# Optimization experiments

Hardware: AMD Instinct MI355X
Metric: run time of the kernel (lower is better)

The kernel has to match this reference:

```python
import jax, jax.numpy as jnp
import numpy as np

D_MODEL = 768
CTX_DIM = 1024
N_HEAD = 12
N_QUERIES = 256
DIM_HEAD = D_MODEL // N_HEAD  # 64
INNER = DIM_HEAD * N_HEAD     # 768
EPS = 1e-5


def layernorm(x, w, b):
    mu = jnp.mean(x, axis=-1, keepdims=True)
    var = jnp.mean((x - mu) ** 2, axis=-1, keepdims=True)
    return (x - mu) * jax.lax.rsqrt(var + EPS) * w + b


def setup_inputs() -> dict:
    key = jax.random.key(0)
    ks = jax.random.split(key, 9)
    x = jax.random.normal(ks[0], (8, 4096, CTX_DIM), dtype=jnp.float32)
    query = jax.random.normal(ks[1], (N_QUERIES, D_MODEL), dtype=jnp.float32)
    # Linear weights stored [in, out] (y = x @ W)
    Wq = jax.random.normal(ks[2], (D_MODEL, INNER), dtype=jnp.float32) * 0.02
    Wkv = jax.random.normal(ks[3], (CTX_DIM, 2 * INNER), dtype=jnp.float32) * 0.02
    Wout = jax.random.normal(ks[4], (INNER, D_MODEL), dtype=jnp.float32) * 0.02
    ln_q_w = jnp.ones((D_MODEL,), jnp.float32)
    ln_q_b = jnp.zeros((D_MODEL,), jnp.float32)
    ln_k_w = jnp.ones((CTX_DIM,), jnp.float32)
    ln_k_b = jnp.zeros((CTX_DIM,), jnp.float32)
    return {"x": x, "query": query, "ln_q_w": ln_q_w, "ln_q_b": ln_q_b,
            "ln_k_w": ln_k_w, "ln_k_b": ln_k_b, "Wq": Wq, "Wkv": Wkv, "Wout": Wout}


def reference(x, query, ln_q_w, ln_q_b, ln_k_w, ln_k_b, Wq, Wkv, Wout):
    b = x.shape[0]
    h, dh = N_HEAD, DIM_HEAD
    scale = dh ** -0.5
    xk = x[:, None]  # b 1 n d  (m = 1)
    m, n = xk.shape[1], xk.shape[2]
    q = jnp.broadcast_to(query, (b, m) + query.shape)  # b m nq d
    xk = layernorm(xk, ln_k_w, ln_k_b)
    q = layernorm(q, ln_q_w, ln_q_b)
    q = q @ Wq                          # b m nq inner
    kv = xk @ Wkv                       # b m n 2*inner
    k, v = jnp.split(kv, 2, axis=-1)
    def split_heads(t):
        bb, tt, nn, _ = t.shape
        return t.reshape(bb, tt, nn, h, dh).transpose(0, 3, 1, 2, 4)  # b h t n dh
    q, k, v = split_heads(q), split_heads(k), split_heads(v)
    sim = jnp.einsum('bhtid,bhtjd->bhtij', q * scale, k)
    attn = jax.nn.softmax(sim, axis=-1)
    out = jnp.einsum('bhtij,bhtjd->bhtid', attn, v)  # b h t nq dh
    out = out.transpose(0, 2, 3, 1, 4).reshape(b, m, N_QUERIES, INNER)
    return (out @ Wout).squeeze(axis=1)  # b nq d_model
```

## Files before the change

### kernel.cpp

```cpp
#include <hip/hip_runtime.h>
#include <hip/hip_bf16.h>
#include <math.h>

#define B_    8
#define T_    4096
#define CD    1024
#define DM    768
#define NH    12
#define DH    64
#define NQ    256
#define INNER 768
#define NKV   1536
#define MKV   (B_*T_)
#define EPS   1e-5f
#define SCALE 0.125f

typedef __attribute__((ext_vector_type(8))) short short8;
typedef __attribute__((ext_vector_type(4))) float f32x4;

__device__ __forceinline__ unsigned short f2bf(float f) {
  union { __hip_bfloat16 h; unsigned short u; } cv;
  cv.h = __float2bfloat16(f);
  return cv.u;
}
__device__ __forceinline__ float bf2f(unsigned short u) {
  return __uint_as_float(((unsigned int)u) << 16);
}

__global__ __launch_bounds__(256) void tbw_kernel(
    const float* __restrict__ s0, unsigned short* __restrict__ d0,
    const float* __restrict__ s1, unsigned short* __restrict__ d1,
    const float* __restrict__ s2, unsigned short* __restrict__ d2) {
  int z = blockIdx.z;
  const float* src; unsigned short* dst; int SR, SC;
  if (z == 0)      { src = s0; dst = d0; SR = CD;    SC = NKV; }
  else if (z == 1) { src = s1; dst = d1; SR = DM;    SC = INNER; }
  else             { src = s2; dst = d2; SR = INNER; SC = DM; }
  int k0 = blockIdx.x * 32, n0 = blockIdx.y * 32;
  if (k0 >= SR || n0 >= SC) return;
  __shared__ float tile[32][33];
  int tid = threadIdx.x;
  int r = tid >> 3, c4 = (tid & 7) * 4;
  float4 v = *reinterpret_cast<const float4*>(&src[(size_t)(k0 + r) * SC + n0 + c4]);
  tile[r][c4 + 0] = v.x; tile[r][c4 + 1] = v.y; tile[r][c4 + 2] = v.z; tile[r][c4 + 3] = v.w;
  __syncthreads();
  ushort4 o4;
  o4.x = f2bf(tile[c4 + 0][r]);
  o4.y = f2bf(tile[c4 + 1][r]);
  o4.z = f2bf(tile[c4 + 2][r]);
  o4.w = f2bf(tile[c4 + 3][r]);
  *reinterpret_cast<ushort4*>(&dst[(size_t)(n0 + r) * SR + k0 + c4]) = o4;
}

__global__ __launch_bounds__(256) void qln_kernel(
    const float* __restrict__ query, const float* __restrict__ lnw,
    const float* __restrict__ lnb, unsigned short* __restrict__ qn) {
  int row = blockIdx.x, tid = threadIdx.x;
  __shared__ float rbuf[256];
  const float* qr = query + (size_t)row * DM;
  float v0 = qr[tid], v1 = qr[tid + 256], v2 = qr[tid + 512];
  rbuf[tid] = v0 + v1 + v2;
  __syncthreads();
  for (int o = 128; o > 0; o >>= 1) { if (tid < o) rbuf[tid] += rbuf[tid + o]; __syncthreads(); }
  float mean = rbuf[0] * (1.f / 768.f);
  __syncthreads();
  float d0 = v0 - mean, d1 = v1 - mean, d2 = v2 - mean;
  rbuf[tid] = d0 * d0 + d1 * d1 + d2 * d2;
  __syncthreads();
  for (int o = 128; o > 0; o >>= 1) { if (tid < o) rbuf[tid] += rbuf[tid + o]; __syncthreads(); }
  float var = rbuf[0] * (1.f / 768.f);
  float rs = rsqrtf(var + EPS);
  unsigned short* dst = qn + (size_t)row * DM;
  dst[tid]       = f2bf(d0 * rs * lnw[tid]       + lnb[tid]);
  dst[tid + 256] = f2bf(d1 * rs * lnw[tid + 256] + lnb[tid + 256]);
  dst[tid + 512] = f2bf(d2 * rs * lnw[tid + 512] + lnb[tid + 512]);
}

__global__ __launch_bounds__(256) void xnorm_kernel(
    const float* __restrict__ x, const float* __restrict__ lnw,
    const float* __restrict__ lnb, unsigned short* __restrict__ xn) {
  int row = blockIdx.x, tid = threadIdx.x;
  float4 v = reinterpret_cast<const float4*>(x + (size_t)row * CD)[tid];
  float s  = v.x + v.y + v.z + v.w;
  float ss = v.x * v.x + v.y * v.y + v.z * v.z + v.w * v.w;
  #pragma unroll
  for (int o = 32; o > 0; o >>= 1) { s += __shfl_down(s, o); ss += __shfl_down(ss, o); }
  __shared__ float sm[8];
  int wid = tid >> 6, lane = tid & 63;
  if (lane == 0) { sm[wid] = s; sm[4 + wid] = ss; }
  __syncthreads();
  float S  = sm[0] + sm[1] + sm[2] + sm[3];
  float SS = sm[4] + sm[5] + sm[6] + sm[7];
  float m  = S * (1.f / 1024.f);
  float var = SS * (1.f / 1024.f) - m * m;
  float rs = rsqrtf(fmaxf(var, 0.f) + EPS);
  float4 wv = reinterpret_cast<const float4*>(lnw)[tid];
  float4 bv = reinterpret_cast<const float4*>(lnb)[tid];
  ushort4 o4;
  o4.x = f2bf((v.x - m) * rs * wv.x + bv.x);
  o4.y = f2bf((v.y - m) * rs * wv.y + bv.y);
  o4.z = f2bf((v.z - m) * rs * wv.z + bv.z);
  o4.w = f2bf((v.w - m) * rs * wv.w + bv.w);
  reinterpret_cast<ushort4*>(xn + (size_t)row * CD)[tid] = o4;
}

template <int MODE>
__global__ __launch_bounds__(256) void gemm128_kernel(
    const unsigned short* __restrict__ A, const unsigned short* __restrict__ Bt,
    void* __restrict__ Cout, int N, int K, int nN, float scale, int swz) {
  __shared__ __attribute__((aligned(16))) unsigned short As[128 * 64];
  __shared__ __attribute__((aligned(16))) unsigned short Bs[128 * 64];
  int tid = threadIdx.x;
  int w = tid >> 6, lane = tid & 63;
  int bid = blockIdx.x;
  int sw = swz ? ((bid & 7) * ((int)gridDim.x >> 3) + (bid >> 3)) : bid;
  int mt = sw / nN, nt = sw % nN;
  int m0 = mt * 128, n0 = nt * 128;

  int srow[4], skoff[4];
  #pragma unroll
  for (int i = 0; i < 4; ++i) {
    int L = w * 4096 + i * 1024 + lane * 16;
    int row = L >> 7;
    int slot = (L >> 4) & 7;
    srow[i] = row;
    skoff[i] = ((slot ^ (row & 7)) << 3);
  }

  f32x4 acc[4][4];
  #pragma unroll
  for (int m = 0; m < 4; ++m)
    #pragma unroll
    for (int n = 0; n < 4; ++n) acc[m][n] = (f32x4){0.f, 0.f, 0.f, 0.f};

  int wr = w >> 1, wc = w & 1;
  int l15 = lane & 15, l4 = lane >> 4;

  for (int t = 0; t < K / 64; ++t) {
    int k0 = t * 64;
    #pragma unroll
    for (int i = 0; i < 4; ++i) {
      __builtin_amdgcn_global_load_lds(
          (const __attribute__((address_space(1))) void*)(A + (size_t)(m0 + srow[i]) * K + k0 + skoff[i]),
          (__attribute__((address_space(3))) void*)(As + w * 2048 + i * 512 + lane * 8),
          16, 0, 0);
    }
    #pragma unroll
    for (int i = 0; i < 4; ++i) {
      __builtin_amdgcn_global_load_lds(
          (const __attribute__((address_space(1))) void*)(Bt + (size_t)(n0 + srow[i]) * K + k0 + skoff[i]),
          (__attribute__((address_space(3))) void*)(Bs + w * 2048 + i * 512 + lane * 8),
          16, 0, 0);
    }
    __syncthreads();
    #pragma unroll
    for (int kh = 0; kh < 2; ++kh) {
      short8 af[4], bf[4];
      #pragma unroll
      for (int m = 0; m < 4; ++m) {
        int row = wr * 64 + m * 16 + l15;
        int byte = row * 128 + (((l4 + 4 * kh) ^ (row & 7)) << 4);
        af[m] = *reinterpret_cast<const short8*>(reinterpret_cast<const char*>(As) + byte);
      }
      #pragma unroll
      for (int n = 0; n < 4; ++n) {
        int row = wc * 64 + n * 16 + l15;
        int byte = row * 128 + (((l4 + 4 * kh) ^ (row & 7)) << 4);
        bf[n] = *reinterpret_cast<const short8*>(reinterpret_cast<const char*>(Bs) + byte);
      }
      #pragma unroll
      for (int m = 0; m < 4; ++m)
        #pragma unroll
        for (int n = 0; n < 4; ++n)
          acc[m][n] = __builtin_amdgcn_mfma_f32_16x16x32_bf16(af[m], bf[n], acc[m][n], 0, 0, 0);
    }
    __syncthreads();
  }

  #pragma unroll
  for (int m = 0; m < 4; ++m) {
    int grow = m0 + wr * 64 + m * 16 + l4 * 4;
    #pragma unroll
    for (int n = 0; n < 4; ++n) {
      int gcol = n0 + wc * 64 + n * 16 + l15;
      #pragma unroll
      for (int r = 0; r < 4; ++r) {
        if (MODE == 0)
          ((unsigned short*)Cout)[(size_t)(grow + r) * N + gcol] = f2bf(acc[m][n][r] * scale);
        else
          ((float*)Cout)[(size_t)(grow + r) * N + gcol] = acc[m][n][r];
      }
    }
  }
}

#define KBM 256
#define KBN 256
#define KBK 64
__global__ __launch_bounds__(512, 2) void kv_split_kernel(
    const unsigned short* __restrict__ xn, const unsigned short* __restrict__ wkvT,
    unsigned short* __restrict__ kvbK, unsigned short* __restrict__ vT) {
  __shared__ __attribute__((aligned(16))) unsigned short As[2][KBM * KBK];
  __shared__ __attribute__((aligned(16))) unsigned short Bs[2][KBN * KBK];
  int tid = threadIdx.x;
  int w = tid >> 6, lane = tid & 63;
  int wm = w >> 2, wn = w & 3;
  int l15 = lane & 15, l4 = lane >> 4;

  int bid = blockIdx.x;
  int sw = (bid & 7) * 96 + (bid >> 3);
  int mt = sw / (NKV / KBN), nt = sw % (NKV / KBN);
  int m0 = mt * KBM, n0 = nt * KBN;

  int srow[4], koff[4];
  #pragma unroll
  for (int i = 0; i < 4; ++i) {
    int r = i * 64 + (tid >> 3);
    srow[i] = r;
    koff[i] = (((tid & 7) ^ (r & 7)) << 3);
  }

  f32x4 acc[8][4];
  #pragma unroll
  for (int m = 0; m < 8; ++m)
    #pragma unroll
    for (int n = 0; n < 4; ++n) acc[m][n] = (f32x4){0.f, 0.f, 0.f, 0.f};

  #pragma unroll
  for (int i = 0; i < 4; ++i) {
    __builtin_amdgcn_global_load_lds(
        (const __attribute__((address_space(1))) void*)(xn + (size_t)(m0 + srow[i]) * CD + koff[i]),
        (__attribute__((address_space(3))) void*)(&As[0][0] + i * 4096 + tid * 8), 16, 0, 0);
    __builtin_amdgcn_global_load_lds(
        (const __attribute__((address_space(1))) void*)(wkvT + (size_t)(n0 + srow[i]) * CD + koff[i]),
        (__attribute__((address_space(3))) void*)(&Bs[0][0] + i * 4096 + tid * 8), 16, 0, 0);
  }
  __syncthreads();

  for (int t = 0; t < CD / KBK; ++t) {
    int cur = t & 1;
    if (t + 1 < CD / KBK) {
      int k0 = (t + 1) * KBK;
      #pragma unroll
      for (int i = 0; i < 4; ++i) {
        __builtin_amdgcn_global_load_lds(
            (const __attribute__((address_space(1))) void*)(xn + (size_t)(m0 + srow[i]) * CD + k0 + koff[i]),
            (__attribute__((address_space(3))) void*)(&As[cur ^ 1][0] + i * 4096 + tid * 8), 16, 0, 0);
        __builtin_amdgcn_global_load_lds(
            (const __attribute__((address_space(1))) void*)(wkvT + (size_t)(n0 + srow[i]) * CD + k0 + koff[i]),
            (__attribute__((address_space(3))) void*)(&Bs[cur ^ 1][0] + i * 4096 + tid * 8), 16, 0, 0);
      }
    }
    const char* Ab = reinterpret_cast<const char*>(&As[cur][0]);
    const char* Bb = reinterpret_cast<const char*>(&Bs[cur][0]);
    #pragma unroll
    for (int kh = 0; kh < 2; ++kh) {
      short8 bf[4];
      #pragma unroll
      for (int n = 0; n < 4; ++n) {
        int row = wn * 64 + n * 16 + l15;
        int byt = row * 128 + (((kh * 4 + l4) ^ (row & 7)) << 4);
        bf[n] = *reinterpret_cast<const short8*>(Bb + byt);
      }
      #pragma unroll
      for (int m = 0; m < 8; ++m) {
        int row = wm * 128 + m * 16 + l15;
        int byt = row * 128 + (((kh * 4 + l4) ^ (row & 7)) << 4);
        short8 af = *reinterpret_cast<const short8*>(Ab + byt);
        #pragma unroll
        for (int n = 0; n < 4; ++n)
          acc[m][n] = __builtin_amdgcn_mfma_f32_16x16x32_bf16(af, bf[n], acc[m][n], 0, 0, 0);
      }
    }
    __syncthreads();
  }

  if (nt < 3) {
    #pragma unroll
    for (int m = 0; m < 8; ++m) {
      int grow = m0 + wm * 128 + m * 16 + l4 * 4;
      #pragma unroll
      for (int n = 0; n < 4; ++n) {
        int gcol = nt * 256 + wn * 64 + n * 16 + l15;
        #pragma unroll
        for (int r = 0; r < 4; ++r)
          kvbK[(size_t)(grow + r) * INNER + gcol] = f2bf(acc[m][n][r]);
      }
    }
  } else {
    int b = m0 >> 12;
    int jblk = m0 & 4095;
    char* Asc = reinterpret_cast<char*>(&As[0][0]);
    char* Bsc = reinterpret_cast<char*>(&Bs[0][0]);
    char* tb = (wn < 2 ? Asc : Bsc) + (wn & 1) * 32768;
    #pragma unroll
    for (int m = 0; m < 8; ++m) {
      int off = (wm * 128 + m * 16 + l4 * 4) * 2;
      #pragma unroll
      for (int n = 0; n < 4; ++n) {
        int d = n * 16 + l15;
        ushort4 o4;
        o4.x = f2bf(acc[m][n][0]); o4.y = f2bf(acc[m][n][1]);
        o4.z = f2bf(acc[m][n][2]); o4.w = f2bf(acc[m][n][3]);
        *reinterpret_cast<ushort4*>(tb + d * 512 + (off ^ ((d & 7) << 4))) = o4;
      }
    }
    __syncthreads();
    #pragma unroll
    for (int e = 0; e < 16; ++e) {
      int lin = e * 8192 + tid * 16;
      int wnn = lin >> 15;
      int rem = lin & 32767;
      int d = rem >> 9;
      int inner = rem & 511;
      short8 v8 = *reinterpret_cast<const short8*>(
          (wnn < 2 ? Asc : Bsc) + (wnn & 1) * 32768 + d * 512 + (inner ^ ((d & 7) << 4)));
      int jl = inner >> 1;
      int hh = (nt - 3) * 4 + wnn;
      unsigned short* dst = vT + ((size_t)(b * NH + hh) * DH + d) * T_ + jblk + jl;
      *reinterpret_cast<short8*>(dst) = v8;
    }
  }
}

__global__ __launch_bounds__(256) void attn_mfma_kernel(
    const unsigned short* __restrict__ qpb, const unsigned short* __restrict__ kvbK,
    const unsigned short* __restrict__ vT,
    unsigned short* __restrict__ pOb, float* __restrict__ pM, float* __restrict__ pL) {
  int bh = blockIdx.x, kc = blockIdx.y, qt = blockIdx.z;
  int b = bh / NH, h = bh % NH;
  __shared__ __attribute__((aligned(16))) unsigned short Ks[2][4096];
  __shared__ __attribute__((aligned(16))) unsigned short Vs[2][4096];
  __shared__ __attribute__((aligned(16))) unsigned short Ps[4][1024];
  int tid = threadIdx.x;
  int w = tid >> 6, lane = tid & 63;
  int l15 = lane & 15, l4 = lane >> 4;

  short8 qf[2];
  {
    const unsigned short* qb = qpb + (size_t)(qt * 64 + w * 16 + l15) * INNER + h * DH;
    qf[0] = *reinterpret_cast<const short8*>(qb + l4 * 8);
    qf[1] = *reinterpret_cast<const short8*>(qb + 32 + l4 * 8);
  }

  int srow0 = w * 16 + (lane >> 3);
  int srow1 = srow0 + 8;
  int koff0 = (((lane & 7) ^ (srow0 & 7)) << 3);
  int koff1 = (((lane & 7) ^ (srow1 & 7)) << 3);

  const size_t kbase = ((size_t)b * T_) * INNER + h * DH;
  const size_t vbase = ((size_t)bh * DH) * T_;

  auto stageKV = [&](int kt, int d) {
    int j0 = kc * 2048 + kt * 64;
    __builtin_amdgcn_global_load_lds(
        (const __attribute__((address_space(1))) void*)(kvbK + kbase + (size_t)(j0 + srow0) * INNER + koff0),
        (__attribute__((address_space(3))) void*)(&Ks[d][0] + w * 1024 + lane * 8), 16, 0, 0);
    __builtin_amdgcn_global_load_lds(
        (const __attribute__((address_space(1))) void*)(kvbK + kbase + (size_t)(j0 + srow1) * INNER + koff1),
        (__attribute__((address_space(3))) void*)(&Ks[d][0] + w * 1024 + 512 + lane * 8), 16, 0, 0);
    __builtin_amdgcn_global_load_lds(
        (const __attribute__((address_space(1))) void*)(vT + vbase + (size_t)srow0 * T_ + j0 + koff0),
        (__attribute__((address_space(3))) void*)(&Vs[d][0] + w * 1024 + lane * 8), 16, 0, 0);
    __builtin_amdgcn_global_load_lds(
        (const __attribute__((address_space(1))) void*)(vT + vbase + (size_t)srow1 * T_ + j0 + koff1),
        (__attribute__((address_space(3))) void*)(&Vs[d][0] + w * 1024 + 512 + lane * 8), 16, 0, 0);
  };

  f32x4 o[4];
  #pragma unroll
  for (int i = 0; i < 4; ++i) o[i] = (f32x4){0.f, 0.f, 0.f, 0.f};
  float m_run = -1e30f, l_run = 0.f;

  stageKV(0, 0);

  for (int kt = 0; kt < 32; ++kt) {
    int cur = kt & 1;
    if (kt + 1 < 32) {
      stageKV(kt + 1, cur ^ 1);
      asm volatile("s_waitcnt vmcnt(4)" ::: "memory");
    } else {
      asm volatile("s_waitcnt vmcnt(0)" ::: "memory");
    }
    __builtin_amdgcn_s_barrier();
    __builtin_amdgcn_sched_barrier(0);

    const char* Kb = reinterpret_cast<const char*>(&Ks[cur][0]);
    const char* Vb = reinterpret_cast<const char*>(&Vs[cur][0]);

    f32x4 st[4];
    __builtin_amdgcn_s_setprio(1);
    #pragma unroll
    for (int sub = 0; sub < 4; ++sub) {
      st[sub] = (f32x4){0.f, 0.f, 0.f, 0.f};
      #pragma unroll
      for (int hf = 0; hf < 2; ++hf) {
        int row = sub * 16 + l15;
        int byt = row * 128 + (((l4 + 4 * hf) ^ (row & 7)) << 4);
        short8 kf = *reinterpret_cast<const short8*>(Kb + byt);
        st[sub] = __builtin_amdgcn_mfma_f32_16x16x32_bf16(kf, qf[hf], st[sub], 0, 0, 0);
      }
    }
    __builtin_amdgcn_s_setprio(0);

    float tmax = -1e30f;
    #pragma unroll
    for (int sub = 0; sub < 4; ++sub)
      #pragma unroll
      for (int r = 0; r < 4; ++r) tmax = fmaxf(tmax, st[sub][r]);
    tmax = fmaxf(tmax, __shfl_xor(tmax, 16));
    tmax = fmaxf(tmax, __shfl_xor(tmax, 32));

    if (__ballot(tmax > m_run + 8.f)) {
      float m_new = fmaxf(m_run, tmax);
      float alpha = __expf(m_run - m_new);
      float ao[4];
      #pragma unroll
      for (int r = 0; r < 4; ++r) ao[r] = __shfl(alpha, (l4 << 2) | r);
      #pragma unroll
      for (int ds = 0; ds < 4; ++ds)
        #pragma unroll
        for (int r = 0; r < 4; ++r) o[ds][r] *= ao[r];
      l_run *= alpha;
      m_run = m_new;
    }

    float psum = 0.f;
    #pragma unroll
    for (int sub = 0; sub < 4; ++sub) {
      float p0 = __expf(st[sub][0] - m_run);
      float p1 = __expf(st[sub][1] - m_run);
      float p2 = __expf(st[sub][2] - m_run);
      float p3 = __expf(st[sub][3] - m_run);
      psum += (p0 + p1) + (p2 + p3);
      unsigned int u0 = (unsigned int)f2bf(p0) | ((unsigned int)f2bf(p1) << 16);
      unsigned int u1 = (unsigned int)f2bf(p2) | ((unsigned int)f2bf(p3) << 16);
      int slot = (sub * 2 + (l4 >> 1)) ^ (l15 & 7);
      int byt = l15 * 128 + (slot << 4) + (l4 & 1) * 8;
      uint2 uv; uv.x = u0; uv.y = u1;
      *reinterpret_cast<uint2*>(reinterpret_cast<char*>(Ps[w]) + byt) = uv;
    }
    psum += __shfl_xor(psum, 16);
    psum += __shfl_xor(psum, 32);
    l_run += psum;

    short8 pa[2];
    #pragma unroll
    for (int hf = 0; hf < 2; ++hf) {
      int byt = l15 * 128 + ((((hf << 2) + l4) ^ (l15 & 7)) << 4);
      pa[hf] = *reinterpret_cast<const short8*>(reinterpret_cast<const char*>(Ps[w]) + byt);
    }
    __builtin_amdgcn_s_setprio(1);
    #pragma unroll
    for (int ds = 0; ds < 4; ++ds) {
      #pragma unroll
      for (int hf = 0; hf < 2; ++hf) {
        int row = ds * 16 + l15;
        int byt = row * 128 + (((l4 + 4 * hf) ^ (row & 7)) << 4);
        short8 vf = *reinterpret_cast<const short8*>(Vb + byt);
        o[ds] = __builtin_amdgcn_mfma_f32_16x16x32_bf16(pa[hf], vf, o[ds], 0, 0, 0);
      }
    }
    __builtin_amdgcn_s_setprio(0);
    __builtin_amdgcn_s_barrier();
    __builtin_amdgcn_sched_barrier(0);
  }

  int pidx = bh * 2 + kc;
  int qrow0 = qt * 64 + w * 16;
  if (l4 == 0) {
    pM[(size_t)pidx * NQ + qrow0 + l15] = m_run;
    pL[(size_t)pidx * NQ + qrow0 + l15] = l_run;
  }
  #pragma unroll
  for (int ds = 0; ds < 4; ++ds)
    #pragma unroll
    for (int r = 0; r < 4; ++r)
      pOb[((size_t)pidx * NQ + qrow0 + l4 * 4 + r) * DH + ds * 16 + l15] = f2bf(o[ds][r]);
}

__global__ __launch_bounds__(256) void outfuse_kernel(
    const unsigned short* __restrict__ pOb, const float* __restrict__ pM,
    const float* __restrict__ pL, const unsigned short* __restrict__ WoutT,
    float* __restrict__ out) {
  __shared__ __attribute__((aligned(16))) unsigned short As[128 * 64];
  __shared__ __attribute__((aligned(16))) unsigned short Bs[128 * 64];
  int tid = threadIdx.x;
  int w = tid >> 6, lane = tid & 63;
  int bid = blockIdx.x;
  int sw = (bid & 7) * 12 + (bid >> 3);
  int mt = sw / 6, nt = sw % 6;
  int m0 = mt * 128, n0 = nt * 128;

  int srow[4], skoff[4];
  #pragma unroll
  for (int i = 0; i < 4; ++i) {
    int L = w * 4096 + i * 1024 + lane * 16;
    int row = L >> 7;
    int slot = (L >> 4) & 7;
    srow[i] = row;
    skoff[i] = ((slot ^ (row & 7)) << 3);
  }

  f32x4 acc[4][4];
  #pragma unroll
  for (int m = 0; m < 4; ++m)
    #pragma unroll
    for (int n = 0; n < 4; ++n) acc[m][n] = (f32x4){0.f, 0.f, 0.f, 0.f};

  int wr = w >> 1, wc = w & 1;
  int l15 = lane & 15, l4 = lane >> 4;

  for (int t = 0; t < NH; ++t) {
    #pragma unroll
    for (int i = 0; i < 4; ++i) {
      int lin = i * 256 + tid;
      int r = lin >> 3, sl = lin & 7;
      int gr = m0 + r;
      int b = gr >> 8, q = gr & 255;
      size_t i0 = ((size_t)(b * NH + t) * 2) * NQ + q;
      size_t i1 = i0 + NQ;
      float m1 = pM[i0], m2 = pM[i1], l1 = pL[i0], l2 = pL[i1];
      float Mx = fmaxf(m1, m2);
      float w1 = __expf(m1 - Mx), w2 = __expf(m2 - Mx);
      float invL = 1.f / (l1 * w1 + l2 * w2);
      w1 *= invL; w2 *= invL;
      short8 s0 = *reinterpret_cast<const short8*>(pOb + i0 * DH + sl * 8);
      short8 s1 = *reinterpret_cast<const short8*>(pOb + i1 * DH + sl * 8);
      short8 v8;
      #pragma unroll
      for (int k = 0; k < 8; ++k)
        v8[k] = (short)f2bf(bf2f((unsigned short)s0[k]) * w1 +
                            bf2f((unsigned short)s1[k]) * w2);
      *reinterpret_cast<short8*>(reinterpret_cast<char*>(As) +
                                 r * 128 + ((sl ^ (r & 7)) << 4)) = v8;
    }
    int k0 = t * 64;
    #pragma unroll
    for (int i = 0; i < 4; ++i) {
      __builtin_amdgcn_global_load_lds(
          (const __attribute__((address_space(1))) void*)(WoutT + (size_t)(n0 + srow[i]) * INNER + k0 + skoff[i]),
          (__attribute__((address_space(3))) void*)(Bs + w * 2048 + i * 512 + lane * 8),
          16, 0, 0);
    }
    __syncthreads();
    #pragma unroll
    for (int kh = 0; kh < 2; ++kh) {
      short8 af[4], bf[4];
      #pragma unroll
      for (int m = 0; m < 4; ++m) {
        int row = wr * 64 + m * 16 + l15;
        int byte = row * 128 + (((l4 + 4 * kh) ^ (row & 7)) << 4);
        af[m] = *reinterpret_cast<const short8*>(reinterpret_cast<const char*>(As) + byte);
      }
      #pragma unroll
      for (int n = 0; n < 4; ++n) {
        int row = wc * 64 + n * 16 + l15;
        int byte = row * 128 + (((l4 + 4 * kh) ^ (row & 7)) << 4);
        bf[n] = *reinterpret_cast<const short8*>(reinterpret_cast<const char*>(Bs) + byte);
      }
      #pragma unroll
      for (int m = 0; m < 4; ++m)
        #pragma unroll
        for (int n = 0; n < 4; ++n)
          acc[m][n] = __builtin_amdgcn_mfma_f32_16x16x32_bf16(af[m], bf[n], acc[m][n], 0, 0, 0);
    }
    __syncthreads();
  }

  #pragma unroll
  for (int m = 0; m < 4; ++m) {
    int grow = m0 + wr * 64 + m * 16 + l4 * 4;
    #pragma unroll
    for (int n = 0; n < 4; ++n) {
      int gcol = n0 + wc * 64 + n * 16 + l15;
      #pragma unroll
      for (int r = 0; r < 4; ++r)
        out[(size_t)(grow + r) * DM + gcol] = acc[m][n][r];
    }
  }
}

extern "C" void kernel_launch(void* const* d_in, const int* in_sizes, int n_in,
                              void* d_out, int out_size, void* d_ws, size_t ws_size,
                              hipStream_t stream) {
  const float* x      = (const float*)d_in[0];
  const float* query  = (const float*)d_in[1];
  const float* ln_q_w = (const float*)d_in[2];
  const float* ln_q_b = (const float*)d_in[3];
  const float* ln_k_w = (const float*)d_in[4];
  const float* ln_k_b = (const float*)d_in[5];
  const float* Wq     = (const float*)d_in[6];
  const float* Wkv    = (const float*)d_in[7];
  const float* Wout   = (const float*)d_in[8];
  float* out = (float*)d_out;

  unsigned short* qpb   = (unsigned short*)d_ws;
  unsigned short* xn    = qpb + (size_t)NQ * INNER;
  unsigned short* wkvT  = xn + (size_t)MKV * CD;
  unsigned short* kvbK  = wkvT + (size_t)NKV * CD;
  unsigned short* vT    = kvbK + (size_t)MKV * INNER;
  unsigned short* pOb   = vT + (size_t)MKV * INNER;
  float* pM    = (float*)(pOb + (size_t)B_ * NH * 2 * NQ * DH);
  float* pL    = pM + (size_t)B_ * NH * 2 * NQ;
  unsigned short* qn    = (unsigned short*)(pL + (size_t)B_ * NH * 2 * NQ);
  unsigned short* WqT   = qn + (size_t)NQ * DM;
  unsigned short* WoutT = WqT + (size_t)DM * INNER;

  hipLaunchKernelGGL(tbw_kernel, dim3(CD / 32, NKV / 32, 3), dim3(256), 0, stream,
                     Wkv, wkvT, Wq, WqT, Wout, WoutT);
  hipLaunchKernelGGL(qln_kernel, dim3(NQ), dim3(256), 0, stream,
                     query, ln_q_w, ln_q_b, qn);
  hipLaunchKernelGGL((gemm128_kernel<0>), dim3((NQ / 128) * (INNER / 128)), dim3(256), 0, stream,
                     qn, WqT, (void*)qpb, INNER, DM, INNER / 128, SCALE, 0);
  hipLaunchKernelGGL(xnorm_kernel, dim3(MKV), dim3(256), 0, stream,
                     x, ln_k_w, ln_k_b, xn);
  hipLaunchKernelGGL(kv_split_kernel, dim3((MKV / KBM) * (NKV / KBN)), dim3(512), 0, stream,
                     xn, wkvT, kvbK, vT);
  hipLaunchKernelGGL(attn_mfma_kernel, dim3(B_ * NH, 2, 4), dim3(256), 0, stream,
                     qpb, kvbK, vT, pOb, pM, pL);
  hipLaunchKernelGGL(outfuse_kernel, dim3((B_ * NQ / 128) * (DM / 128)), dim3(256), 0, stream,
                     pOb, pM, pL, WoutT, out);
}
```

Before: 250.7 us.

## Halve KV GEMM K-tile to shrink LDS, add MFMA priority, two-pass V transpose

```diff
diff --git a/kernel.cpp b/kernel.cpp
--- a/kernel.cpp
+++ b/kernel.cpp
@@ -196,12 +196,12 @@
 
 #define KBM 256
 #define KBN 256
-#define KBK 64
+#define RBK 32
 __global__ __launch_bounds__(512, 2) void kv_split_kernel(
     const unsigned short* __restrict__ xn, const unsigned short* __restrict__ wkvT,
     unsigned short* __restrict__ kvbK, unsigned short* __restrict__ vT) {
-  __shared__ __attribute__((aligned(16))) unsigned short As[2][KBM * KBK];
-  __shared__ __attribute__((aligned(16))) unsigned short Bs[2][KBN * KBK];
+  __shared__ __attribute__((aligned(16))) unsigned short As[2][KBM * RBK];
+  __shared__ __attribute__((aligned(16))) unsigned short Bs[2][KBN * RBK];
   int tid = threadIdx.x;
   int w = tid >> 6, lane = tid & 63;
   int wm = w >> 2, wn = w & 3;
@@ -212,13 +212,28 @@
   int mt = sw / (NKV / KBN), nt = sw % (NKV / KBN);
   int m0 = mt * KBM, n0 = nt * KBN;
 
-  int srow[4], koff[4];
-  #pragma unroll
-  for (int i = 0; i < 4; ++i) {
-    int r = i * 64 + (tid >> 3);
-    srow[i] = r;
-    koff[i] = (((tid & 7) ^ (r & 7)) << 3);
-  }
+  int sr0 = tid >> 2;
+  int sr1 = 128 + (tid >> 2);
+  int sk0 = (((tid & 3) ^ ((sr0 >> 2) & 3)) << 3);
+  int sk1 = (((tid & 3) ^ ((sr1 >> 2) & 3)) << 3);
+
+  auto stage = [&](int t) {
+    int d = t & 1;
+    const unsigned short* sa = xn + (size_t)m0 * CD + t * RBK;
+    const unsigned short* sb = wkvT + (size_t)n0 * CD + t * RBK;
+    __builtin_amdgcn_global_load_lds(
+        (const __attribute__((address_space(1))) void*)(sa + (size_t)sr0 * CD + sk0),
+        (__attribute__((address_space(3))) void*)(&As[d][0] + tid * 8), 16, 0, 0);
+    __builtin_amdgcn_global_load_lds(
+        (const __attribute__((address_space(1))) void*)(sa + (size_t)sr1 * CD + sk1),
+        (__attribute__((address_space(3))) void*)(&As[d][4096] + tid * 8), 16, 0, 0);
+    __builtin_amdgcn_global_load_lds(
+        (const __attribute__((address_space(1))) void*)(sb + (size_t)sr0 * CD + sk0),
+        (__attribute__((address_space(3))) void*)(&Bs[d][0] + tid * 8), 16, 0, 0);
+    __builtin_amdgcn_global_load_lds(
+        (const __attribute__((address_space(1))) void*)(sb + (size_t)sr1 * CD + sk1),
+        (__attribute__((address_space(3))) void*)(&Bs[d][4096] + tid * 8), 16, 0, 0);
+  };
 
   f32x4 acc[8][4];
   #pragma unroll
@@ -226,52 +241,30 @@
     #pragma unroll
     for (int n = 0; n < 4; ++n) acc[m][n] = (f32x4){0.f, 0.f, 0.f, 0.f};
 
-  #pragma unroll
-  for (int i = 0; i < 4; ++i) {
-    __builtin_amdgcn_global_load_lds(
-        (const __attribute__((address_space(1))) void*)(xn + (size_t)(m0 + srow[i]) * CD + koff[i]),
-        (__attribute__((address_space(3))) void*)(&As[0][0] + i * 4096 + tid * 8), 16, 0, 0);
-    __builtin_amdgcn_global_load_lds(
-        (const __attribute__((address_space(1))) void*)(wkvT + (size_t)(n0 + srow[i]) * CD + koff[i]),
-        (__attribute__((address_space(3))) void*)(&Bs[0][0] + i * 4096 + tid * 8), 16, 0, 0);
-  }
+  stage(0);
   __syncthreads();
 
-  for (int t = 0; t < CD / KBK; ++t) {
+  for (int t = 0; t < CD / RBK; ++t) {
     int cur = t & 1;
-    if (t + 1 < CD / KBK) {
-      int k0 = (t + 1) * KBK;
-      #pragma unroll
-      for (int i = 0; i < 4; ++i) {
-        __builtin_amdgcn_global_load_lds(
-            (const __attribute__((address_space(1))) void*)(xn + (size_t)(m0 + srow[i]) * CD + k0 + koff[i]),
-            (__attribute__((address_space(3))) void*)(&As[cur ^ 1][0] + i * 4096 + tid * 8), 16, 0, 0);
-        __builtin_amdgcn_global_load_lds(
-            (const __attribute__((address_space(1))) void*)(wkvT + (size_t)(n0 + srow[i]) * CD + k0 + koff[i]),
-            (__attribute__((address_space(3))) void*)(&Bs[cur ^ 1][0] + i * 4096 + tid * 8), 16, 0, 0);
-      }
-    }
+    if (t + 1 < CD / RBK) stage(t + 1);
     const char* Ab = reinterpret_cast<const char*>(&As[cur][0]);
     const char* Bb = reinterpret_cast<const char*>(&Bs[cur][0]);
-    #pragma unroll
-    for (int kh = 0; kh < 2; ++kh) {
-      short8 bf[4];
-      #pragma unroll
-      for (int n = 0; n < 4; ++n) {
-        int row = wn * 64 + n * 16 + l15;
-        int byt = row * 128 + (((kh * 4 + l4) ^ (row & 7)) << 4);
-        bf[n] = *reinterpret_cast<const short8*>(Bb + byt);
-      }
-      #pragma unroll
-      for (int m = 0; m < 8; ++m) {
-        int row = wm * 128 + m * 16 + l15;
-        int byt = row * 128 + (((kh * 4 + l4) ^ (row & 7)) << 4);
-        short8 af = *reinterpret_cast<const short8*>(Ab + byt);
-        #pragma unroll
-        for (int n = 0; n < 4; ++n)
-          acc[m][n] = __builtin_amdgcn_mfma_f32_16x16x32_bf16(af, bf[n], acc[m][n], 0, 0, 0);
-      }
-    }
+    short8 bf[4];
+    #pragma unroll
+    for (int n = 0; n < 4; ++n) {
+      int row = wn * 64 + n * 16 + l15;
+      bf[n] = *reinterpret_cast<const short8*>(Bb + row * 64 + ((l4 ^ ((row >> 2) & 3)) << 4));
+    }
+    __builtin_amdgcn_s_setprio(1);
+    #pragma unroll
+    for (int m = 0; m < 8; ++m) {
+      int row = wm * 128 + m * 16 + l15;
+      short8 af = *reinterpret_cast<const short8*>(Ab + row * 64 + ((l4 ^ ((row >> 2) & 3)) << 4));
+      #pragma unroll
+      for (int n = 0; n < 4; ++n)
+        acc[m][n] = __builtin_amdgcn_mfma_f32_16x16x32_bf16(af, bf[n], acc[m][n], 0, 0, 0);
+    }
+    __builtin_amdgcn_s_setprio(0);
     __syncthreads();
   }
 
@@ -292,33 +285,39 @@
     int jblk = m0 & 4095;
     char* Asc = reinterpret_cast<char*>(&As[0][0]);
     char* Bsc = reinterpret_cast<char*>(&Bs[0][0]);
-    char* tb = (wn < 2 ? Asc : Bsc) + (wn & 1) * 32768;
-    #pragma unroll
-    for (int m = 0; m < 8; ++m) {
-      int off = (wm * 128 + m * 16 + l4 * 4) * 2;
-      #pragma unroll
-      for (int n = 0; n < 4; ++n) {
-        int d = n * 16 + l15;
-        ushort4 o4;
-        o4.x = f2bf(acc[m][n][0]); o4.y = f2bf(acc[m][n][1]);
-        o4.z = f2bf(acc[m][n][2]); o4.w = f2bf(acc[m][n][3]);
-        *reinterpret_cast<ushort4*>(tb + d * 512 + (off ^ ((d & 7) << 4))) = o4;
-      }
-    }
-    __syncthreads();
-    #pragma unroll
-    for (int e = 0; e < 16; ++e) {
-      int lin = e * 8192 + tid * 16;
-      int wnn = lin >> 15;
-      int rem = lin & 32767;
-      int d = rem >> 9;
-      int inner = rem & 511;
-      short8 v8 = *reinterpret_cast<const short8*>(
-          (wnn < 2 ? Asc : Bsc) + (wnn & 1) * 32768 + d * 512 + (inner ^ ((d & 7) << 4)));
-      int jl = inner >> 1;
-      int hh = (nt - 3) * 4 + wnn;
-      unsigned short* dst = vT + ((size_t)(b * NH + hh) * DH + d) * T_ + jblk + jl;
-      *reinterpret_cast<short8*>(dst) = v8;
+    #pragma unroll
+    for (int p = 0; p < 2; ++p) {
+      if ((wn >> 1) == p) {
+        char* tb = (wn & 1) ? Bsc : Asc;
+        #pragma unroll
+        for (int m = 0; m < 8; ++m) {
+          int off = (wm * 128 + m * 16 + l4 * 4) * 2;
+          #pragma unroll
+          for (int n = 0; n < 4; ++n) {
+            int d = n * 16 + l15;
+            ushort4 o4;
+            o4.x = f2bf(acc[m][n][0]); o4.y = f2bf(acc[m][n][1]);
+            o4.z = f2bf(acc[m][n][2]); o4.w = f2bf(acc[m][n][3]);
+            *reinterpret_cast<ushort4*>(tb + d * 512 + (off ^ ((d & 7) << 4))) = o4;
+          }
+        }
+      }
+      __syncthreads();
+      #pragma unroll
+      for (int e = 0; e < 8; ++e) {
+        int lin = e * 8192 + tid * 16;
+        int wnn = lin >> 15;
+        int rem = lin & 32767;
+        int d = rem >> 9;
+        int inner = rem & 511;
+        short8 v8 = *reinterpret_cast<const short8*>(
+            (wnn ? Bsc : Asc) + d * 512 + (inner ^ ((d & 7) << 4)));
+        int jl = inner >> 1;
+        int hh = (nt - 3) * 4 + p * 2 + wnn;
+        unsigned short* dst = vT + ((size_t)(b * NH + hh) * DH + d) * T_ + jblk + jl;
+        *reinterpret_cast<short8*>(dst) = v8;
+      }
+      __syncthreads();
     }
   }
 }
```

Measured after the change: 281.5 us. +12.3%, slower.
